# Optimization experiments

Measured on AMD Instinct MI355X. Metric: run time of the kernel, lower is better.

Reference implementation:

```python
import jax, jax.numpy as jnp
import numpy as np
from jax import lax

EMB, HDIM, OBS_LEN = 64, 64, 8
BATCH, NSCENES, SCENE = 32768, 4096, 8
SEQ_LEN = 12


def setup_inputs() -> dict:
    key = jax.random.key(0)
    ks = jax.random.split(key, 16)
    obs_traj = jax.random.normal(ks[0], (OBS_LEN, BATCH, 2), jnp.float32)
    last_pos = jax.random.normal(ks[1], (BATCH, 2), jnp.float32)
    last_pos_rel = jax.random.normal(ks[2], (BATCH, 2), jnp.float32)
    starts = jnp.arange(NSCENES, dtype=jnp.int32) * SCENE
    seq_start_end = jnp.stack([starts, starts + SCENE], axis=1)  # (NSCENES, 2)
    # spatial_embedding: Linear(2, EMB)
    W_se = jax.random.normal(ks[3], (EMB, 2), jnp.float32) * 0.5
    b_se = jax.random.normal(ks[4], (EMB,), jnp.float32) * 0.1
    # weight-normed convs: w = g * v / ||v||_(in,k) per out-channel, bias init zero
    def conv_params(k, cout, cin, ksz):
        ka, kb = jax.random.split(k)
        std = np.sqrt(4.0 / (ksz * cin))
        v = jax.random.normal(ka, (cout, cin, ksz), jnp.float32) * std
        g = jax.random.uniform(kb, (cout,), jnp.float32, 0.5, 1.5)
        b = jnp.zeros((cout,), jnp.float32)
        return v, g, b
    v1, g1, b1 = conv_params(ks[5], HDIM, EMB, 3)
    v2, g2, b2 = conv_params(ks[6], HDIM // 2, HDIM, 3)
    v3, g3, b3 = conv_params(ks[7], HDIM // 2, HDIM // 2, 3)
    # hidden2pos: Linear(2*HDIM, 2)
    W_hp = jax.random.normal(ks[8], (2, 2 * HDIM), jnp.float32) * 0.05
    b_hp = jax.random.normal(ks[9], (2,), jnp.float32) * 0.05
    return {"obs_traj": obs_traj, "last_pos": last_pos, "last_pos_rel": last_pos_rel,
            "W_se": W_se, "b_se": b_se,
            "v1": v1, "g1": g1, "b1": b1,
            "v2": v2, "g2": g2, "b2": b2,
            "v3": v3, "g3": g3, "b3": b3,
            "W_hp": W_hp, "b_hp": b_hp,
            "seq_start_end": seq_start_end, "seq_len": SEQ_LEN}


def _wn_conv_relu(x, v, g, b):
    # weight-norm: w[o] = g[o] * v[o] / ||v[o]||  (norm over in-channels and kernel)
    norm = jnp.sqrt(jnp.sum(v * v, axis=(1, 2)))
    w = v * (g / norm)[:, None, None]
    y = lax.conv_general_dilated(x, w, (1,), 'VALID',
                                 dimension_numbers=('NCH', 'OIH', 'NCH'))
    return jax.nn.relu(y + b[None, :, None])


def reference(obs_traj, last_pos, last_pos_rel,
              W_se, b_se, v1, g1, b1, v2, g2, b2, v3, g3, b3, W_hp, b_hp,
              seq_start_end, seq_len):
    batch = last_pos.shape[0]
    nseg = seq_start_end.shape[0]
    h_dim = v1.shape[0]
    # scene id for each pedestrian (segments are contiguous [start,end) ranges)
    seg = jnp.searchsorted(seq_start_end[:, 0], jnp.arange(batch), side='right') - 1
    # obs_traj embedding -> (batch, EMB, OBS_LEN)
    emb = obs_traj @ W_se.T + b_se            # (T, B, EMB)
    obs_emb0 = jnp.transpose(emb, (1, 2, 0))  # (B, EMB, T)

    def step(carry, _):
        obs_emb, lp = carry
        s = _wn_conv_relu(obs_emb, v1, g1, b1)   # (B, H, T-2)
        s = _wn_conv_relu(s, v2, g2, b2)         # (B, H/2, T-4)
        s = _wn_conv_relu(s, v3, g3, b3)         # (B, H/2, T-6)
        s = s.reshape(batch, h_dim)              # (H/2)*(T-6) == H
        mx = jax.ops.segment_max(s, seg, num_segments=nseg)  # ragged per-scene max
        st = jnp.concatenate([s, mx[seg]], axis=1)           # (B, 2H)
        rel = st @ W_hp.T + b_hp                 # (B, 2)
        lp = rel + lp
        dec = rel @ W_se.T + b_se                # (B, EMB)
        obs_emb = jnp.concatenate([obs_emb[:, :, 1:], dec[:, :, None]], axis=2)
        return (obs_emb, lp), rel

    _, rels = lax.scan(step, (obs_emb0, last_pos), None, length=seq_len)
    return rels  # (seq_len, batch, 2)
```

## Files before the change

kernel.cpp:

```cpp
#include <hip/hip_runtime.h>

#define BATCH 32768
#define SEQLEN 12
#define NBLK 512

typedef short short8 __attribute__((ext_vector_type(8)));
typedef float f32x4 __attribute__((ext_vector_type(4)));
typedef unsigned short ushort_t;

static __device__ __forceinline__ unsigned short f2bf(float x) {
    unsigned u = __float_as_uint(x);
    return (unsigned short)((u + 0x7FFFu + ((u >> 16) & 1u)) >> 16);
}
static __device__ __forceinline__ float bf2f(unsigned short h) {
    return __uint_as_float(((unsigned)h) << 16);
}

#define MFMA __builtin_amdgcn_mfma_f32_16x16x32_bf16


#define C1PED(PX, PY, QX, QY, RX, RY, PPED) do {                              \
    float v_ = cK1;                                                           \
    v_ = fmaf(ccA0, PX, v_); v_ = fmaf(ccB0, PY, v_);                         \
    v_ = fmaf(ccA1, QX, v_); v_ = fmaf(ccB1, QY, v_);                         \
    v_ = fmaf(ccA2, RX, v_); v_ = fmaf(ccB2, RY, v_);                         \
    v_ = fmaxf(v_, 0.f);                                                      \
    ushort_t h_ = f2bf(v_);                                                   \
    s1sh[wv][PPED][lane] = h_;                                                \
    s1sl[wv][PPED][lane] = f2bf(v_ - bf2f(h_));                               \
} while(0)

#define S1_FRAGREAD(SL) do {                                                  \
    s1fh[SL][0] = *(const short8*)&s1sh[wv][n][kg*8];                         \
    s1fh[SL][1] = *(const short8*)&s1sh[wv][n][32 + kg*8];                    \
    s1fl[SL][0] = *(const short8*)&s1sl[wv][n][kg*8];                         \
    s1fl[SL][1] = *(const short8*)&s1sl[wv][n][32 + kg*8];                    \
} while(0)

#define CONV1COL(SA, SB, SC, SL) do {                                         \
    _Pragma("unroll")                                                         \
    for (int pp_ = 0; pp_ < 8; ++pp_) {                                       \
        float4 fa_ = *(const float4*)&pos_s[wv][SA][2*pp_][0];                \
        float4 fb_ = *(const float4*)&pos_s[wv][SB][2*pp_][0];                \
        float4 fc_ = *(const float4*)&pos_s[wv][SC][2*pp_][0];                \
        C1PED(fa_.x, fa_.y, fb_.x, fb_.y, fc_.x, fc_.y, 2*pp_);               \
        C1PED(fa_.z, fa_.w, fb_.z, fb_.w, fc_.z, fc_.w, 2*pp_+1);             \
    }                                                                         \
    S1_FRAGREAD(SL);                                                          \
} while(0)

#define CONV2COL(CM3) do {                                                    \
    _Pragma("unroll")                                                         \
    for (int T = 0; T < 2; ++T) {                                             \
        f32x4 a1 = {0.f,0.f,0.f,0.f}, a2 = {0.f,0.f,0.f,0.f},                 \
              a3 = {0.f,0.f,0.f,0.f};                                         \
        _Pragma("unroll")                                                     \
        for (int kb = 0; kb < 6; ++kb) {                                      \
            const int sl = ((CM3) + (kb >> 1)) % 3, ich = kb & 1;             \
            a1 = MFMA(c2h[T][kb], s1fh[sl][ich], a1, 0, 0, 0);                \
            a2 = MFMA(c2h[T][kb], s1fl[sl][ich], a2, 0, 0, 0);                \
            a3 = MFMA(c2l[T][kb], s1fh[sl][ich], a3, 0, 0, 0);                \
        }                                                                     \
        const float4 bb = *(const float4*)&b2s[T*16 + kg*4];                  \
        float w0 = fmaxf(a1[0]+a2[0]+a3[0]+bb.x, 0.f);                        \
        float w1 = fmaxf(a1[1]+a2[1]+a3[1]+bb.y, 0.f);                        \
        float w2 = fmaxf(a1[2]+a2[2]+a3[2]+bb.z, 0.f);                        \
        float w3 = fmaxf(a1[3]+a2[3]+a3[3]+bb.w, 0.f);                        \
        ushort_t h0=f2bf(w0), h1=f2bf(w1), h2=f2bf(w2), h3=f2bf(w3);          \
        *(uint2*)&s2sh[wv][CM3][n][T*16 + kg*4] = make_uint2(                 \
            (unsigned)h0 | ((unsigned)h1 << 16),                              \
            (unsigned)h2 | ((unsigned)h3 << 16));                             \
        *(uint2*)&s2sl[wv][CM3][n][T*16 + kg*4] = make_uint2(                 \
            (unsigned)f2bf(w0-bf2f(h0)) | ((unsigned)f2bf(w1-bf2f(h1)) << 16),\
            (unsigned)f2bf(w2-bf2f(h2)) | ((unsigned)f2bf(w3-bf2f(h3)) << 16));\
    }                                                                         \
} while(0)

#define CONV3COL(VM3, PARI) do {                                              \
    short8 sbh_[3], sbl_[3];                                                  \
    _Pragma("unroll")                                                         \
    for (int kb = 0; kb < 3; ++kb) {                                          \
        const int sl = ((VM3) + kb) % 3;                                      \
        sbh_[kb] = *(const short8*)&s2sh[wv][sl][n][kg*8];                    \
        sbl_[kb] = *(const short8*)&s2sl[wv][sl][n][kg*8];                    \
    }                                                                         \
    _Pragma("unroll")                                                         \
    for (int T = 0; T < 2; ++T) {                                             \
        f32x4 a1 = {0.f,0.f,0.f,0.f}, a2 = {0.f,0.f,0.f,0.f},                 \
              a3 = {0.f,0.f,0.f,0.f};                                         \
        _Pragma("unroll")                                                     \
        for (int kb = 0; kb < 3; ++kb) {                                      \
            const short8 wh = *(const short8*)&c3wh[T*3+kb][lane][0];         \
            const short8 wl = *(const short8*)&c3wl[T*3+kb][lane][0];         \
            a1 = MFMA(wh, sbh_[kb], a1, 0, 0, 0);                             \
            a2 = MFMA(wh, sbl_[kb], a2, 0, 0, 0);                             \
            a3 = MFMA(wl, sbh_[kb], a3, 0, 0, 0);                             \
        }                                                                     \
        const float4 b3v = *(const float4*)&b3s[T*16 + kg*4];                 \
        float m0 = fmaxf(a1[0]+a2[0]+a3[0]+b3v.x, 0.f);                       \
        float m1 = fmaxf(a1[1]+a2[1]+a3[1]+b3v.y, 0.f);                       \
        float m2 = fmaxf(a1[2]+a2[2]+a3[2]+b3v.z, 0.f);                       \
        float m3 = fmaxf(a1[3]+a2[3]+a3[3]+b3v.w, 0.f);                       \
        c3c[PARI][T] = (f32x4){m0, m1, m2, m3};                               \
        _Pragma("unroll")                                                     \
        for (int msk = 1; msk <= 4; msk <<= 1) {                              \
            m0 = fmaxf(m0, __shfl_xor(m0, msk));                              \
            m1 = fmaxf(m1, __shfl_xor(m1, msk));                              \
            m2 = fmaxf(m2, __shfl_xor(m2, msk));                              \
            m3 = fmaxf(m3, __shfl_xor(m3, msk));                              \
        }                                                                     \
        mxc[PARI][T] = (f32x4){m0, m1, m2, m3};                               \
    }                                                                         \
} while(0)

#define STAGE2(T0) do {                                                       \
    const int tau_ = (T0) + (lane >> 5);                                      \
    const int p_ = (lane >> 1) & 15, c_ = lane & 1;                           \
    pos_s[wv][tau_ & 3][p_][c_] =                                             \
        obs[(size_t)(tau_*BATCH + bped + p_)*2 + c_];                         \
} while(0)

#define STEP(K) do {                                                          \
    const int st = sbase + (K);                                               \
    float pv0a = 0.f, pv0b = 0.f, pv1a = 0.f, pv1b = 0.f;                     \
    {                                                                         \
        const float4* wq = (const float4*)&whp_s[kg][0];                      \
        _Pragma("unroll")                                                     \
        for (int q = 0; q < 16; ++q) {                                        \
            float4 ww = wq[q];                                                \
            _Pragma("unroll")                                                 \
            for (int e = 0; e < 4; ++e) {                                     \
                const int j2 = (q & 7)*4 + e;                                 \
                const int jj = j2 & 15;                                       \
                const int T = jj >> 3, r = (jj >> 1) & 3, col = jj & 1;       \
                const int par = col ? (((K)+1) & 1) : ((K) & 1);              \
                float val = (j2 < 16) ? c3c[par][T][r] : mxc[par][T][r];      \
                float wv_ = (e==0)?ww.x:(e==1)?ww.y:(e==2)?ww.z:ww.w;         \
                if (q < 8) { if (q & 1) pv0b = fmaf(wv_, val, pv0b);          \
                             else       pv0a = fmaf(wv_, val, pv0a); }        \
                else       { if (q & 1) pv1b = fmaf(wv_, val, pv1b);          \
                             else       pv1a = fmaf(wv_, val, pv1a); }        \
            }                                                                 \
        }                                                                     \
    }                                                                         \
    float pv0 = pv0a + pv0b, pv1 = pv1a + pv1b;                               \
    pv0 += __shfl_xor(pv0, 16); pv0 += __shfl_xor(pv0, 32);                   \
    pv1 += __shfl_xor(pv1, 16); pv1 += __shfl_xor(pv1, 32);                   \
    const float r0 = pv0 + bhp0, r1 = pv1 + bhp1;                             \
    if (lane < 16) {                                                          \
        float2 o; o.x = r0; o.y = r1;                                         \
        *(float2*)&out[(size_t)(st*BATCH + bped + lane)*2] = o;               \
    }                                                                         \
    if (st < SEQLEN-1) {                                                      \
        if (lane < 16) {                                                      \
            float2 o2; o2.x = r0; o2.y = r1;                                  \
            *(float2*)&pos_s[wv][st & 3][lane][0] = o2;         \
        }                                                                     \
        CONV1COL((st+2)&3, (st+3)&3, st&3, (K)%3);              \
        CONV2COL(((K)+1)%3);                                    \
        CONV3COL(((K)+2)%3, (K)&1);                             \
    }                                                                         \
} while(0)

__global__ __launch_bounds__(256, 1)
void enc_wp(const float* __restrict__ obs,
            const float* __restrict__ Wse, const float* __restrict__ bse,
            const float* __restrict__ v1, const float* __restrict__ g1, const float* __restrict__ b1,
            const float* __restrict__ v2, const float* __restrict__ g2, const float* __restrict__ b2,
            const float* __restrict__ v3, const float* __restrict__ g3, const float* __restrict__ b3,
            const float* __restrict__ Whp, const float* __restrict__ bhp,
            float* __restrict__ out)
{
    __shared__ __align__(16) ushort_t s1sh[4][16][72], s1sl[4][16][72];
    __shared__ __align__(16) ushort_t s2sh[4][3][16][40], s2sl[4][3][16][40];
    __shared__ __align__(16) float    pos_s[4][4][16][2];
    __shared__ __align__(16) float    whp_s[4][68];
    __shared__ __align__(16) ushort_t c3wh[6][64][8], c3wl[6][64][8];
    __shared__ __align__(16) float    b2s[32], b3s[32];

    const int tid  = threadIdx.x;
    const int wv   = tid >> 6;
    const int lane = tid & 63;
    const int n    = lane & 15, kg = lane >> 4;
    const int bped = (blockIdx.x*4 + wv)*16;

    float* scr   = (float*)&s2sh[0][0][0][0];
    float* wse_s = scr;
    float* bse_s = scr + 128;
    float* sc2_s = scr + 192;
    float* sc3_s = scr + 224;

    if (wv == 0) {
        wse_s[lane] = Wse[lane]; wse_s[64 + lane] = Wse[64 + lane];
        bse_s[lane] = bse[lane];
        if (lane < 32) {
            b2s[lane] = b2[lane];
            const float* v = v2 + lane*192; float s = 0.f;
            for (int j = 0; j < 192; ++j) s += v[j]*v[j];
            sc2_s[lane] = g2[lane] / sqrtf(s);
        } else {
            b3s[lane-32] = b3[lane-32];
            const float* v = v3 + (lane-32)*96; float s = 0.f;
            for (int j = 0; j < 96; ++j) s += v[j]*v[j];
            sc3_s[lane-32] = g3[lane-32] / sqrtf(s);
        }
        #pragma unroll
        for (int q = 0; q < 4; ++q) {
            int d = lane >> 5, jp = lane & 31, jj = jp & 15;
            int T = jj >> 3, r = (jj >> 1) & 3, col = jj & 1;
            int off = (T*16 + q*4 + r)*2 + col + ((jp >= 16) ? 64 : 0);
            whp_s[q][lane] = Whp[d*128 + off];
        }
    }
    __syncthreads();

    float ccA0, ccA1, ccA2, ccB0, ccB1, ccB2, cK1;
    {
        const float* v = v1 + lane*192; float s = 0.f;
        for (int j = 0; j < 192; ++j) s += v[j]*v[j];
        const float sc1 = g1[lane] / sqrtf(s);
        float dA0=0,dA1=0,dA2=0,dB0=0,dB1=0,dB2=0,dC0=0,dC1=0,dC2=0;
        const float* vr = v1 + lane*192;
        #pragma unroll 4
        for (int ic = 0; ic < 64; ++ic) {
            float w0 = vr[ic*3], w1 = vr[ic*3+1], w2 = vr[ic*3+2];
            float we0 = wse_s[ic*2], we1 = wse_s[ic*2+1], be = bse_s[ic];
            dA0 = fmaf(w0, we0, dA0); dB0 = fmaf(w0, we1, dB0); dC0 = fmaf(w0, be, dC0);
            dA1 = fmaf(w1, we0, dA1); dB1 = fmaf(w1, we1, dB1); dC1 = fmaf(w1, be, dC1);
            dA2 = fmaf(w2, we0, dA2); dB2 = fmaf(w2, we1, dB2); dC2 = fmaf(w2, be, dC2);
        }
        ccA0 = sc1*dA0; ccA1 = sc1*dA1; ccA2 = sc1*dA2;
        ccB0 = sc1*dB0; ccB1 = sc1*dB1; ccB2 = sc1*dB2;
        cK1  = fmaf(sc1, (dC0 + dC1) + dC2, b1[lane]);
    }
    short8 c2h[2][6], c2l[2][6];
    #pragma unroll
    for (int T = 0; T < 2; ++T) {
        const int oc2 = T*16 + n;
        const float s2s = sc2_s[oc2];
        #pragma unroll
        for (int kb = 0; kb < 6; ++kb) {
            const int tap = kb >> 1, ich = kb & 1;
            #pragma unroll
            for (int j = 0; j < 8; ++j) {
                const int ic = ich*32 + kg*8 + j;
                float w = v2[(size_t)(oc2*64 + ic)*3 + tap] * s2s;
                ushort_t hb = f2bf(w);
                c2h[T][kb][j] = (short)hb;
                c2l[T][kb][j] = (short)f2bf(w - bf2f(hb));
            }
        }
    }
    if (wv == 1) {
        #pragma unroll
        for (int f = 0; f < 6; ++f) {
            const int T = f / 3, kb = f % 3;
            const int oc = T*16 + n;
            const float s3s = sc3_s[oc];
            #pragma unroll
            for (int j = 0; j < 8; ++j) {
                const int ic = kg*8 + j;
                float w = v3[(size_t)(oc*32 + ic)*3 + kb] * s3s;
                ushort_t hb = f2bf(w);
                c3wh[f][lane][j] = hb;
                c3wl[f][lane][j] = f2bf(w - bf2f(hb));
            }
        }
    }
    const float bhp0 = bhp[0], bhp1 = bhp[1];
    __syncthreads();

    short8 s1fh[3][2], s1fl[3][2];
    f32x4 c3c[2][2], mxc[2][2];

    STAGE2(0); STAGE2(2);
    CONV1COL(0, 1, 2, 0);
    CONV1COL(1, 2, 3, 1);
    STAGE2(4);
    CONV1COL(2, 3, 0, 2);
    CONV2COL(0);
    CONV1COL(3, 0, 1, 0);
    CONV2COL(1);
    STAGE2(6);
    CONV1COL(0, 1, 2, 1);
    CONV2COL(2);
    CONV3COL(0, 0);
    CONV1COL(1, 2, 3, 2);
    CONV2COL(0);
    CONV3COL(1, 1);

    #pragma unroll 1
    for (int hh = 0; hh < 2; ++hh) {
        const int sbase = hh * 6;
        STEP(0); STEP(1); STEP(2); STEP(3); STEP(4); STEP(5);
    }
}

extern "C" void kernel_launch(void* const* d_in, const int* in_sizes, int n_in,
                              void* d_out, int out_size, void* d_ws, size_t ws_size,
                              hipStream_t stream)
{
    const float* obs = (const float*)d_in[0];
    const float* Wse = (const float*)d_in[3];
    const float* bse = (const float*)d_in[4];
    const float* v1  = (const float*)d_in[5];
    const float* g1  = (const float*)d_in[6];
    const float* b1  = (const float*)d_in[7];
    const float* v2  = (const float*)d_in[8];
    const float* g2  = (const float*)d_in[9];
    const float* b2  = (const float*)d_in[10];
    const float* v3  = (const float*)d_in[11];
    const float* g3  = (const float*)d_in[12];
    const float* b3  = (const float*)d_in[13];
    const float* Whp = (const float*)d_in[14];
    const float* bhp = (const float*)d_in[15];

    enc_wp<<<NBLK, 256, 0, stream>>>(obs, Wse, bse, v1, g1, b1, v2, g2, b2,
                                     v3, g3, b3, Whp, bhp, (float*)d_out);
}
```

Measured before the change: 206.9 us.

## Move conv2 weights to LDS, keep conv3 inputs in registers, allow two blocks per CU

Conv2 hi/lo bf16 weight fragments move out of per-thread registers into shared memory, and only the conv3 low-part weights stay in registers. The conv2 output ring buffer in LDS shrinks to one slot because each column's fragment is read back into registers right after it is written. The launch bound is raised to 2 blocks per CU. The aim is to cut VGPR pressure and LDS footprint so occupancy doubles, at the cost of extra LDS reads inside the MFMA loop.

Result: faster. 175.2 us (-15.3%).

```diff
diff --git a/kernel.cpp b/kernel.cpp
--- a/kernel.cpp
+++ b/kernel.cpp
@@ -57,9 +57,11 @@
         _Pragma("unroll")                                                     \
         for (int kb = 0; kb < 6; ++kb) {                                      \
             const int sl = ((CM3) + (kb >> 1)) % 3, ich = kb & 1;             \
-            a1 = MFMA(c2h[T][kb], s1fh[sl][ich], a1, 0, 0, 0);                \
-            a2 = MFMA(c2h[T][kb], s1fl[sl][ich], a2, 0, 0, 0);                \
-            a3 = MFMA(c2l[T][kb], s1fh[sl][ich], a3, 0, 0, 0);                \
+            const short8 wh = *(const short8*)&c2wh[T*6+kb][lane][0];         \
+            const short8 wl = *(const short8*)&c2wl[T*6+kb][lane][0];         \
+            a1 = MFMA(wh, s1fh[sl][ich], a1, 0, 0, 0);                        \
+            a2 = MFMA(wh, s1fl[sl][ich], a2, 0, 0, 0);                        \
+            a3 = MFMA(wl, s1fh[sl][ich], a3, 0, 0, 0);                        \
         }                                                                     \
         const float4 bb = *(const float4*)&b2s[T*16 + kg*4];                  \
         float w0 = fmaxf(a1[0]+a2[0]+a3[0]+bb.x, 0.f);                        \
@@ -67,34 +69,29 @@
         float w2 = fmaxf(a1[2]+a2[2]+a3[2]+bb.z, 0.f);                        \
         float w3 = fmaxf(a1[3]+a2[3]+a3[3]+bb.w, 0.f);                        \
         ushort_t h0=f2bf(w0), h1=f2bf(w1), h2=f2bf(w2), h3=f2bf(w3);          \
-        *(uint2*)&s2sh[wv][CM3][n][T*16 + kg*4] = make_uint2(                 \
+        *(uint2*)&s2sh[wv][n][T*16 + kg*4] = make_uint2(                      \
             (unsigned)h0 | ((unsigned)h1 << 16),                              \
             (unsigned)h2 | ((unsigned)h3 << 16));                             \
-        *(uint2*)&s2sl[wv][CM3][n][T*16 + kg*4] = make_uint2(                 \
+        *(uint2*)&s2sl[wv][n][T*16 + kg*4] = make_uint2(                      \
             (unsigned)f2bf(w0-bf2f(h0)) | ((unsigned)f2bf(w1-bf2f(h1)) << 16),\
             (unsigned)f2bf(w2-bf2f(h2)) | ((unsigned)f2bf(w3-bf2f(h3)) << 16));\
     }                                                                         \
+    s2fh[(CM3)] = *(const short8*)&s2sh[wv][n][kg*8];                         \
+    s2fl[(CM3)] = *(const short8*)&s2sl[wv][n][kg*8];                         \
 } while(0)
 
 #define CONV3COL(VM3, PARI) do {                                              \
-    short8 sbh_[3], sbl_[3];                                                  \
-    _Pragma("unroll")                                                         \
-    for (int kb = 0; kb < 3; ++kb) {                                          \
-        const int sl = ((VM3) + kb) % 3;                                      \
-        sbh_[kb] = *(const short8*)&s2sh[wv][sl][n][kg*8];                    \
-        sbl_[kb] = *(const short8*)&s2sl[wv][sl][n][kg*8];                    \
-    }                                                                         \
     _Pragma("unroll")                                                         \
     for (int T = 0; T < 2; ++T) {                                             \
         f32x4 a1 = {0.f,0.f,0.f,0.f}, a2 = {0.f,0.f,0.f,0.f},                 \
               a3 = {0.f,0.f,0.f,0.f};                                         \
         _Pragma("unroll")                                                     \
         for (int kb = 0; kb < 3; ++kb) {                                      \
+            const int sl = ((VM3) + kb) % 3;                                  \
             const short8 wh = *(const short8*)&c3wh[T*3+kb][lane][0];         \
-            const short8 wl = *(const short8*)&c3wl[T*3+kb][lane][0];         \
-            a1 = MFMA(wh, sbh_[kb], a1, 0, 0, 0);                             \
-            a2 = MFMA(wh, sbl_[kb], a2, 0, 0, 0);                             \
-            a3 = MFMA(wl, sbh_[kb], a3, 0, 0, 0);                             \
+            a1 = MFMA(wh, s2fh[sl], a1, 0, 0, 0);                             \
+            a2 = MFMA(wh, s2fl[sl], a2, 0, 0, 0);                             \
+            a3 = MFMA(c3l[T][kb], s2fh[sl], a3, 0, 0, 0);                     \
         }                                                                     \
         const float4 b3v = *(const float4*)&b3s[T*16 + kg*4];                 \
         float m0 = fmaxf(a1[0]+a2[0]+a3[0]+b3v.x, 0.f);                       \
@@ -162,7 +159,7 @@
     }                                                                         \
 } while(0)
 
-__global__ __launch_bounds__(256, 1)
+__global__ __launch_bounds__(256, 2)
 void enc_wp(const float* __restrict__ obs,
             const float* __restrict__ Wse, const float* __restrict__ bse,
             const float* __restrict__ v1, const float* __restrict__ g1, const float* __restrict__ b1,
@@ -172,10 +169,11 @@
             float* __restrict__ out)
 {
     __shared__ __align__(16) ushort_t s1sh[4][16][72], s1sl[4][16][72];
-    __shared__ __align__(16) ushort_t s2sh[4][3][16][40], s2sl[4][3][16][40];
+    __shared__ __align__(16) ushort_t s2sh[4][16][40], s2sl[4][16][40];
     __shared__ __align__(16) float    pos_s[4][4][16][2];
     __shared__ __align__(16) float    whp_s[4][68];
-    __shared__ __align__(16) ushort_t c3wh[6][64][8], c3wl[6][64][8];
+    __shared__ __align__(16) ushort_t c2wh[12][64][8], c2wl[12][64][8];
+    __shared__ __align__(16) ushort_t c3wh[6][64][8];
     __shared__ __align__(16) float    b2s[32], b3s[32];
 
     const int tid  = threadIdx.x;
@@ -184,7 +182,7 @@
     const int n    = lane & 15, kg = lane >> 4;
     const int bped = (blockIdx.x*4 + wv)*16;
 
-    float* scr   = (float*)&s2sh[0][0][0][0];
+    float* scr   = (float*)&s1sh[0][0][0];
     float* wse_s = scr;
     float* bse_s = scr + 128;
     float* sc2_s = scr + 192;
@@ -213,6 +211,35 @@
         }
     }
     __syncthreads();
+
+    if (wv == 0) {
+        #pragma unroll
+        for (int f = 0; f < 12; ++f) {
+            const int T = f / 6, kb = f % 6;
+            const int oc = T*16 + n, tap = kb >> 1, ich = kb & 1;
+            const float s2s = sc2_s[oc];
+            #pragma unroll
+            for (int j = 0; j < 8; ++j) {
+                const int ic = ich*32 + kg*8 + j;
+                float w = v2[(size_t)(oc*64 + ic)*3 + tap] * s2s;
+                ushort_t hb = f2bf(w);
+                c2wh[f][lane][j] = hb;
+                c2wl[f][lane][j] = f2bf(w - bf2f(hb));
+            }
+        }
+    } else if (wv == 1) {
+        #pragma unroll
+        for (int f = 0; f < 6; ++f) {
+            const int T = f / 3, kb = f % 3;
+            const int oc = T*16 + n;
+            const float s3s = sc3_s[oc];
+            #pragma unroll
+            for (int j = 0; j < 8; ++j) {
+                const int ic = kg*8 + j;
+                c3wh[f][lane][j] = f2bf(v3[(size_t)(oc*32 + ic)*3 + kb] * s3s);
+            }
+        }
+    }
 
     float ccA0, ccA1, ccA2, ccB0, ccB1, ccB2, cK1;
     {
@@ -233,44 +260,25 @@
         ccB0 = sc1*dB0; ccB1 = sc1*dB1; ccB2 = sc1*dB2;
         cK1  = fmaf(sc1, (dC0 + dC1) + dC2, b1[lane]);
     }
-    short8 c2h[2][6], c2l[2][6];
+    short8 c3l[2][3];
     #pragma unroll
     for (int T = 0; T < 2; ++T) {
-        const int oc2 = T*16 + n;
-        const float s2s = sc2_s[oc2];
+        const int oc = T*16 + n;
+        const float s3s = sc3_s[oc];
         #pragma unroll
-        for (int kb = 0; kb < 6; ++kb) {
-            const int tap = kb >> 1, ich = kb & 1;
-            #pragma unroll
-            for (int j = 0; j < 8; ++j) {
-                const int ic = ich*32 + kg*8 + j;
-                float w = v2[(size_t)(oc2*64 + ic)*3 + tap] * s2s;
-                ushort_t hb = f2bf(w);
-                c2h[T][kb][j] = (short)hb;
-                c2l[T][kb][j] = (short)f2bf(w - bf2f(hb));
-            }
-        }
-    }
-    if (wv == 1) {
-        #pragma unroll
-        for (int f = 0; f < 6; ++f) {
-            const int T = f / 3, kb = f % 3;
-            const int oc = T*16 + n;
-            const float s3s = sc3_s[oc];
+        for (int kb = 0; kb < 3; ++kb) {
             #pragma unroll
             for (int j = 0; j < 8; ++j) {
                 const int ic = kg*8 + j;
                 float w = v3[(size_t)(oc*32 + ic)*3 + kb] * s3s;
-                ushort_t hb = f2bf(w);
-                c3wh[f][lane][j] = hb;
-                c3wl[f][lane][j] = f2bf(w - bf2f(hb));
+                c3l[T][kb][j] = (short)f2bf(w - bf2f(f2bf(w)));
             }
         }
     }
     const float bhp0 = bhp[0], bhp1 = bhp[1];
     __syncthreads();
 
-    short8 s1fh[3][2], s1fl[3][2];
+    short8 s1fh[3][2], s1fl[3][2], s2fh[3], s2fl[3];
     f32x4 c3c[2][2], mxc[2][2];
 
     STAGE2(0); STAGE2(2);
```

## Keep conv2 outputs in register ring and raise occupancy to two blocks/CU

Applied to the files above, without the earlier changes.

Conv2 output columns are now written to a single LDS slot per wave and immediately read back into a 3-deep register ring (s2fh/s2fl), shrinking the s2 LDS buffers. Conv3 reads activations from these registers instead of reloading three columns from LDS. Empty asm barriers on LDS base pointers keep the compiler from hoisting weight and bias loads into long-lived registers, and the conv3 weight preparation is moved earlier because the scratch area now aliases s1sh. Launch bounds go from 1 to 2 blocks per CU to raise occupancy, at the cost of tighter register limits and possible spilling.

Measured after the change: 192.6 us. 6.9% less time.

```diff
diff --git a/kernel.cpp b/kernel.cpp
--- a/kernel.cpp
+++ b/kernel.cpp
@@ -50,6 +50,8 @@
 } while(0)
 
 #define CONV2COL(CM3) do {                                                    \
+    const float* b2b_ = &b2s[0];                                              \
+    asm volatile("" : "+v"(b2b_));                                            \
     _Pragma("unroll")                                                         \
     for (int T = 0; T < 2; ++T) {                                             \
         f32x4 a1 = {0.f,0.f,0.f,0.f}, a2 = {0.f,0.f,0.f,0.f},                 \
@@ -61,42 +63,43 @@
             a2 = MFMA(c2h[T][kb], s1fl[sl][ich], a2, 0, 0, 0);                \
             a3 = MFMA(c2l[T][kb], s1fh[sl][ich], a3, 0, 0, 0);                \
         }                                                                     \
-        const float4 bb = *(const float4*)&b2s[T*16 + kg*4];                  \
+        const float4 bb = *(const float4*)&b2b_[T*16 + kg*4];                 \
         float w0 = fmaxf(a1[0]+a2[0]+a3[0]+bb.x, 0.f);                        \
         float w1 = fmaxf(a1[1]+a2[1]+a3[1]+bb.y, 0.f);                        \
         float w2 = fmaxf(a1[2]+a2[2]+a3[2]+bb.z, 0.f);                        \
         float w3 = fmaxf(a1[3]+a2[3]+a3[3]+bb.w, 0.f);                        \
         ushort_t h0=f2bf(w0), h1=f2bf(w1), h2=f2bf(w2), h3=f2bf(w3);          \
-        *(uint2*)&s2sh[wv][CM3][n][T*16 + kg*4] = make_uint2(                 \
+        *(uint2*)&s2sh[wv][n][T*16 + kg*4] = make_uint2(                      \
             (unsigned)h0 | ((unsigned)h1 << 16),                              \
             (unsigned)h2 | ((unsigned)h3 << 16));                             \
-        *(uint2*)&s2sl[wv][CM3][n][T*16 + kg*4] = make_uint2(                 \
+        *(uint2*)&s2sl[wv][n][T*16 + kg*4] = make_uint2(                      \
             (unsigned)f2bf(w0-bf2f(h0)) | ((unsigned)f2bf(w1-bf2f(h1)) << 16),\
             (unsigned)f2bf(w2-bf2f(h2)) | ((unsigned)f2bf(w3-bf2f(h3)) << 16));\
     }                                                                         \
+    s2fh[(CM3)] = *(const short8*)&s2sh[wv][n][kg*8];                         \
+    s2fl[(CM3)] = *(const short8*)&s2sl[wv][n][kg*8];                         \
 } while(0)
 
 #define CONV3COL(VM3, PARI) do {                                              \
-    short8 sbh_[3], sbl_[3];                                                  \
-    _Pragma("unroll")                                                         \
-    for (int kb = 0; kb < 3; ++kb) {                                          \
-        const int sl = ((VM3) + kb) % 3;                                      \
-        sbh_[kb] = *(const short8*)&s2sh[wv][sl][n][kg*8];                    \
-        sbl_[kb] = *(const short8*)&s2sl[wv][sl][n][kg*8];                    \
-    }                                                                         \
+    const ushort_t* c3hb_ = &c3wh[0][0][0];                                   \
+    const ushort_t* c3lb_ = &c3wl[0][0][0];                                   \
+    asm volatile("" : "+v"(c3hb_), "+v"(c3lb_));                              \
+    const float* b3b_ = &b3s[0];                                              \
+    asm volatile("" : "+v"(b3b_));                                            \
     _Pragma("unroll")                                                         \
     for (int T = 0; T < 2; ++T) {                                             \
         f32x4 a1 = {0.f,0.f,0.f,0.f}, a2 = {0.f,0.f,0.f,0.f},                 \
               a3 = {0.f,0.f,0.f,0.f};                                         \
         _Pragma("unroll")                                                     \
         for (int kb = 0; kb < 3; ++kb) {                                      \
-            const short8 wh = *(const short8*)&c3wh[T*3+kb][lane][0];         \
-            const short8 wl = *(const short8*)&c3wl[T*3+kb][lane][0];         \
-            a1 = MFMA(wh, sbh_[kb], a1, 0, 0, 0);                             \
-            a2 = MFMA(wh, sbl_[kb], a2, 0, 0, 0);                             \
-            a3 = MFMA(wl, sbh_[kb], a3, 0, 0, 0);                             \
-        }                                                                     \
-        const float4 b3v = *(const float4*)&b3s[T*16 + kg*4];                 \
+            const int sl = ((VM3) + kb) % 3;                                  \
+            const short8 wh = *(const short8*)&c3hb_[((T*3+kb)*64+lane)*8];   \
+            const short8 wl = *(const short8*)&c3lb_[((T*3+kb)*64+lane)*8];   \
+            a1 = MFMA(wh, s2fh[sl], a1, 0, 0, 0);                             \
+            a2 = MFMA(wh, s2fl[sl], a2, 0, 0, 0);                             \
+            a3 = MFMA(wl, s2fh[sl], a3, 0, 0, 0);                             \
+        }                                                                     \
+        const float4 b3v = *(const float4*)&b3b_[T*16 + kg*4];                \
         float m0 = fmaxf(a1[0]+a2[0]+a3[0]+b3v.x, 0.f);                       \
         float m1 = fmaxf(a1[1]+a2[1]+a3[1]+b3v.y, 0.f);                       \
         float m2 = fmaxf(a1[2]+a2[2]+a3[2]+b3v.z, 0.f);                       \
@@ -124,22 +127,28 @@
     const int st = sbase + (K);                                               \
     float pv0a = 0.f, pv0b = 0.f, pv1a = 0.f, pv1b = 0.f;                     \
     {                                                                         \
-        const float4* wq = (const float4*)&whp_s[kg][0];                      \
+        const float* wb_ = &whp_s[kg][0];                                     \
         _Pragma("unroll")                                                     \
-        for (int q = 0; q < 16; ++q) {                                        \
-            float4 ww = wq[q];                                                \
+        for (int ch = 0; ch < 4; ++ch) {                                      \
+            asm volatile("" : "+v"(wb_));                                     \
+            const float4* wq = (const float4*)wb_;                            \
             _Pragma("unroll")                                                 \
-            for (int e = 0; e < 4; ++e) {                                     \
-                const int j2 = (q & 7)*4 + e;                                 \
-                const int jj = j2 & 15;                                       \
-                const int T = jj >> 3, r = (jj >> 1) & 3, col = jj & 1;       \
-                const int par = col ? (((K)+1) & 1) : ((K) & 1);              \
-                float val = (j2 < 16) ? c3c[par][T][r] : mxc[par][T][r];      \
-                float wv_ = (e==0)?ww.x:(e==1)?ww.y:(e==2)?ww.z:ww.w;         \
-                if (q < 8) { if (q & 1) pv0b = fmaf(wv_, val, pv0b);          \
-                             else       pv0a = fmaf(wv_, val, pv0a); }        \
-                else       { if (q & 1) pv1b = fmaf(wv_, val, pv1b);          \
-                             else       pv1a = fmaf(wv_, val, pv1a); }        \
+            for (int qq = 0; qq < 4; ++qq) {                                  \
+                const int q = ch*4 + qq;                                      \
+                float4 ww = wq[q];                                            \
+                _Pragma("unroll")                                             \
+                for (int e = 0; e < 4; ++e) {                                 \
+                    const int j2 = (q & 7)*4 + e;                             \
+                    const int jj = j2 & 15;                                   \
+                    const int T = jj >> 3, r = (jj >> 1) & 3, col = jj & 1;   \
+                    const int par = col ? (((K)+1) & 1) : ((K) & 1);          \
+                    float val = (j2 < 16) ? c3c[par][T][r] : mxc[par][T][r];  \
+                    float wv_ = (e==0)?ww.x:(e==1)?ww.y:(e==2)?ww.z:ww.w;     \
+                    if (q < 8) { if (q & 1) pv0b = fmaf(wv_, val, pv0b);      \
+                                 else       pv0a = fmaf(wv_, val, pv0a); }    \
+                    else       { if (q & 1) pv1b = fmaf(wv_, val, pv1b);      \
+                                 else       pv1a = fmaf(wv_, val, pv1a); }    \
+                }                                                             \
             }                                                                 \
         }                                                                     \
     }                                                                         \
@@ -162,7 +171,7 @@
     }                                                                         \
 } while(0)
 
-__global__ __launch_bounds__(256, 1)
+__global__ __launch_bounds__(256, 2)
 void enc_wp(const float* __restrict__ obs,
             const float* __restrict__ Wse, const float* __restrict__ bse,
             const float* __restrict__ v1, const float* __restrict__ g1, const float* __restrict__ b1,
@@ -172,7 +181,7 @@
             float* __restrict__ out)
 {
     __shared__ __align__(16) ushort_t s1sh[4][16][72], s1sl[4][16][72];
-    __shared__ __align__(16) ushort_t s2sh[4][3][16][40], s2sl[4][3][16][40];
+    __shared__ __align__(16) ushort_t s2sh[4][16][40], s2sl[4][16][40];
     __shared__ __align__(16) float    pos_s[4][4][16][2];
     __shared__ __align__(16) float    whp_s[4][68];
     __shared__ __align__(16) ushort_t c3wh[6][64][8], c3wl[6][64][8];
@@ -184,7 +193,7 @@
     const int n    = lane & 15, kg = lane >> 4;
     const int bped = (blockIdx.x*4 + wv)*16;
 
-    float* scr   = (float*)&s2sh[0][0][0][0];
+    float* scr   = (float*)&s1sh[0][0][0];
     float* wse_s = scr;
     float* bse_s = scr + 128;
     float* sc2_s = scr + 192;
@@ -213,6 +222,23 @@
         }
     }
     __syncthreads();
+
+    if (wv == 1) {
+        #pragma unroll
+        for (int f = 0; f < 6; ++f) {
+            const int T = f / 3, kb = f % 3;
+            const int oc = T*16 + n;
+            const float s3s = sc3_s[oc];
+            #pragma unroll
+            for (int j = 0; j < 8; ++j) {
+                const int ic = kg*8 + j;
+                float w = v3[(size_t)(oc*32 + ic)*3 + kb] * s3s;
+                ushort_t hb = f2bf(w);
+                c3wh[f][lane][j] = hb;
+                c3wl[f][lane][j] = f2bf(w - bf2f(hb));
+            }
+        }
+    }
 
     float ccA0, ccA1, ccA2, ccB0, ccB1, ccB2, cK1;
     {
@@ -251,26 +277,10 @@
             }
         }
     }
-    if (wv == 1) {
-        #pragma unroll
-        for (int f = 0; f < 6; ++f) {
-            const int T = f / 3, kb = f % 3;
-            const int oc = T*16 + n;
-            const float s3s = sc3_s[oc];
-            #pragma unroll
-            for (int j = 0; j < 8; ++j) {
-                const int ic = kg*8 + j;
-                float w = v3[(size_t)(oc*32 + ic)*3 + kb] * s3s;
-                ushort_t hb = f2bf(w);
-                c3wh[f][lane][j] = hb;
-                c3wl[f][lane][j] = f2bf(w - bf2f(hb));
-            }
-        }
-    }
     const float bhp0 = bhp[0], bhp1 = bhp[1];
     __syncthreads();
 
-    short8 s1fh[3][2], s1fl[3][2];
+    short8 s1fh[3][2], s1fl[3][2], s2fh[3], s2fl[3];
     f32x4 c3c[2][2], mxc[2][2];
 
     STAGE2(0); STAGE2(2);
```
